# Kernel tuning notes

Hardware: AMD Instinct MI355X
Metric: run time of the kernel (lower is better)

The kernel has to match this reference:

```python
import jax, jax.numpy as jnp
import numpy as np

NH = 16   # num_heads
HD = 128  # head_dim
HS = 2048 # hidden_size
LI, LT = 2048, 512
MLP = 4 * HS


def _ln(x, s, b):
    m = jnp.mean(x, axis=-1, keepdims=True)
    v = jnp.var(x, axis=-1, keepdims=True)
    return (x - m) * jax.lax.rsqrt(v + 1e-6) * s + b


def _rms(x, s):
    return x * jax.lax.rsqrt(jnp.mean(x * x, axis=-1, keepdims=True) + 1e-6) * s


def _mod6(vec, w, b):
    a = (jax.nn.silu(vec) @ w + b)[:, None, :]
    return jnp.split(a, 6, axis=-1)  # shift1,scale1,gate1,shift2,scale2,gate2


def _rope(x, pe):
    B, H, L, D = x.shape
    xr = x.reshape(B, H, L, D // 2, 1, 2)
    return (pe[..., 0] * xr[..., 0] + pe[..., 1] * xr[..., 1]).reshape(B, H, L, D)


def _attention(q, k, v, pe):
    q = _rope(q, pe)
    k = _rope(k, pe)
    scores = jnp.einsum('bhqd,bhkd->bhqk', q, k) * (q.shape[-1] ** -0.5)
    p = jax.nn.softmax(scores, axis=-1)
    o = jnp.einsum('bhqk,bhkd->bhqd', p, v)
    B, H, L, D = o.shape
    return o.transpose(0, 2, 1, 3).reshape(B, L, H * D)


def _prenorm_qkv(x, shift, scale, ln_s, ln_b, qkv_w, qkv_b, qn, kn):
    xm = (1.0 + scale) * _ln(x, ln_s, ln_b) + shift
    y = xm @ qkv_w + qkv_b
    B, L, _ = y.shape
    y = y.reshape(B, L, 3, NH, HD).transpose(2, 0, 3, 1, 4)  # K B H L D
    q, k, v = y[0], y[1], y[2]
    return _rms(q, qn), _rms(k, kn), v


def _forward(img, txt, vec, pe,
             img_mod_w, img_mod_b, img_norm1_s, img_norm1_b, img_qkv_w, img_qkv_b,
             img_qn_s, img_kn_s, img_proj_w, img_proj_b, img_norm2_s, img_norm2_b,
             img_mlp_w1, img_mlp_b1, img_mlp_w2, img_mlp_b2,
             txt_mod_w, txt_mod_b, txt_norm1_s, txt_norm1_b, txt_qkv_w, txt_qkv_b,
             txt_qn_s, txt_kn_s, txt_proj_w, txt_proj_b, txt_norm2_s, txt_norm2_b,
             txt_mlp_w1, txt_mlp_b1, txt_mlp_w2, txt_mlp_b2):
    i_sh1, i_sc1, i_g1, i_sh2, i_sc2, i_g2 = _mod6(vec, img_mod_w, img_mod_b)
    t_sh1, t_sc1, t_g1, t_sh2, t_sc2, t_g2 = _mod6(vec, txt_mod_w, txt_mod_b)

    iq, ik, iv = _prenorm_qkv(img, i_sh1, i_sc1, img_norm1_s, img_norm1_b,
                              img_qkv_w, img_qkv_b, img_qn_s, img_kn_s)
    tq, tk, tv = _prenorm_qkv(txt, t_sh1, t_sc1, txt_norm1_s, txt_norm1_b,
                              txt_qkv_w, txt_qkv_b, txt_qn_s, txt_kn_s)

    q = jnp.concatenate((tq, iq), axis=2)
    k = jnp.concatenate((tk, ik), axis=2)
    v = jnp.concatenate((tv, iv), axis=2)
    attn = _attention(q, k, v, pe)  # [B, LT+LI, HS]
    Lt = txt.shape[1]
    txt_attn, img_attn = attn[:, :Lt], attn[:, Lt:]

    img = img + i_g1 * (img_attn @ img_proj_w + img_proj_b)
    img_h = (1.0 + i_sc2) * _ln(img, img_norm2_s, img_norm2_b) + i_sh2
    img = img + i_g2 * (jax.nn.gelu(img_h @ img_mlp_w1 + img_mlp_b1) @ img_mlp_w2 + img_mlp_b2)

    txt = txt + t_g1 * (txt_attn @ txt_proj_w + txt_proj_b)
    txt_h = (1.0 + t_sc2) * _ln(txt, txt_norm2_s, txt_norm2_b) + t_sh2
    txt = txt + t_g2 * (jax.nn.gelu(txt_h @ txt_mlp_w1 + txt_mlp_b1) @ txt_mlp_w2 + txt_mlp_b2)
    return img, txt


def setup_inputs() -> dict:
    key = jax.random.key(0)
    ki = iter(jax.random.split(key, 48))
    def n(shape, s=0.02):
        return jax.random.normal(next(ki), shape, jnp.float32) * s
    d = {
        'img': jax.random.normal(next(ki), (1, LI, HS), jnp.float32),
        'txt': jax.random.normal(next(ki), (1, LT, HS), jnp.float32),
        'vec': jax.random.normal(next(ki), (1, HS), jnp.float32),
        'pe': jax.random.normal(next(ki), (1, 1, LT + LI, HD // 2, 2, 2), jnp.float32),
    }
    for p in ('img', 'txt'):
        d[p + '_mod_w'] = n((HS, 6 * HS)); d[p + '_mod_b'] = jnp.zeros((6 * HS,), jnp.float32)
        d[p + '_norm1_s'] = jnp.ones((HS,), jnp.float32); d[p + '_norm1_b'] = jnp.zeros((HS,), jnp.float32)
        d[p + '_qkv_w'] = n((HS, 3 * HS)); d[p + '_qkv_b'] = jnp.zeros((3 * HS,), jnp.float32)
        d[p + '_qn_s'] = jnp.ones((HD,), jnp.float32); d[p + '_kn_s'] = jnp.ones((HD,), jnp.float32)
        d[p + '_proj_w'] = n((HS, HS)); d[p + '_proj_b'] = jnp.zeros((HS,), jnp.float32)
        d[p + '_norm2_s'] = jnp.ones((HS,), jnp.float32); d[p + '_norm2_b'] = jnp.zeros((HS,), jnp.float32)
        d[p + '_mlp_w1'] = n((HS, MLP)); d[p + '_mlp_b1'] = jnp.zeros((MLP,), jnp.float32)
        d[p + '_mlp_w2'] = n((MLP, HS)); d[p + '_mlp_b2'] = jnp.zeros((HS,), jnp.float32)
    return d


def reference(img, txt, vec, pe,
              img_mod_w, img_mod_b, img_norm1_s, img_norm1_b, img_qkv_w, img_qkv_b,
              img_qn_s, img_kn_s, img_proj_w, img_proj_b, img_norm2_s, img_norm2_b,
              img_mlp_w1, img_mlp_b1, img_mlp_w2, img_mlp_b2,
              txt_mod_w, txt_mod_b, txt_norm1_s, txt_norm1_b, txt_qkv_w, txt_qkv_b,
              txt_qn_s, txt_kn_s, txt_proj_w, txt_proj_b, txt_norm2_s, txt_norm2_b,
              txt_mlp_w1, txt_mlp_b1, txt_mlp_w2, txt_mlp_b2):
    return _forward(img, txt, vec, pe,
                    img_mod_w, img_mod_b, img_norm1_s, img_norm1_b, img_qkv_w, img_qkv_b,
                    img_qn_s, img_kn_s, img_proj_w, img_proj_b, img_norm2_s, img_norm2_b,
                    img_mlp_w1, img_mlp_b1, img_mlp_w2, img_mlp_b2,
                    txt_mod_w, txt_mod_b, txt_norm1_s, txt_norm1_b, txt_qkv_w, txt_qkv_b,
                    txt_qn_s, txt_kn_s, txt_proj_w, txt_proj_b, txt_norm2_s, txt_norm2_b,
                    txt_mlp_w1, txt_mlp_b1, txt_mlp_w2, txt_mlp_b2)
```

## Files before the change

### kernel.cpp

```cpp
#include <hip/hip_runtime.h>
#include <hip/hip_bf16.h>
#include <math.h>

typedef __bf16 bf16;
typedef __bf16 bf16x2 __attribute__((ext_vector_type(2)));
typedef __bf16 bf16x4 __attribute__((ext_vector_type(4)));
typedef __bf16 bf16x8 __attribute__((ext_vector_type(8)));
typedef float f32x4 __attribute__((ext_vector_type(4)));

#define HS 2048
#define NH 16
#define HD 128
#define LT 512
#define LI 2048
#define LQ 2560
#define MLP_D 8192
#define SPLIT 4
#define KVS (LQ / SPLIT)
#define KVBLK 32
#define NTILES (KVS / KVBLK)

__device__ __forceinline__ f32x4 mfma16(bf16x8 a, bf16x8 b, f32x4 c) {
  return __builtin_amdgcn_mfma_f32_16x16x32_bf16(a, b, c, 0, 0, 0);
}

__device__ __forceinline__ void gl_lds16(const bf16* g, bf16* l) {
  __builtin_amdgcn_global_load_lds((const __attribute__((address_space(1))) void*)g,
                                   (__attribute__((address_space(3))) void*)l, 16, 0, 0);
}

__global__ void k_silu(const float* __restrict__ v, float* __restrict__ s) {
  int i = blockIdx.x * 256 + threadIdx.x;
  float x = v[i];
  s[i] = x / (1.f + expf(-x));
}

__global__ __launch_bounds__(256) void k_mod_partial(
    const float* __restrict__ s, const float* __restrict__ w_txt,
    const float* __restrict__ w_img, float* __restrict__ part) {
  int strm = blockIdx.x / 48;
  int n = (blockIdx.x % 48) * 256 + threadIdx.x;
  const float* w = strm ? w_img : w_txt;
  int k0 = blockIdx.y * 256;
  __shared__ float sl[256];
  sl[threadIdx.x] = s[k0 + threadIdx.x];
  __syncthreads();
  float acc = 0.f;
  for (int k = 0; k < 256; k++)
    acc += sl[k] * w[(size_t)(k0 + k) * 12288 + n];
  part[((size_t)blockIdx.y * 2 + strm) * 12288 + n] = acc;
}

__global__ __launch_bounds__(256) void k_mod_reduce(
    const float* __restrict__ part, const float* __restrict__ b_txt,
    const float* __restrict__ b_img, float* __restrict__ mod) {
  int strm = blockIdx.x / 48;
  int n = (blockIdx.x % 48) * 256 + threadIdx.x;
  float acc = strm ? b_img[n] : b_txt[n];
  for (int kc = 0; kc < 8; kc++)
    acc += part[((size_t)kc * 2 + strm) * 12288 + n];
  mod[(size_t)strm * 12288 + n] = acc;
}

__global__ __launch_bounds__(256) void k_transpose_cvt(
    const float* __restrict__ src, bf16* __restrict__ dst, int R, int C) {
  __shared__ float t[64][65];
  int tx = threadIdx.x & 63, ty = threadIdx.x >> 6;
  int c0 = blockIdx.x * 64, r0 = blockIdx.y * 64;
  for (int i = 0; i < 64; i += 4)
    t[ty + i][tx] = src[(size_t)(r0 + ty + i) * C + c0 + tx];
  __syncthreads();
#pragma unroll
  for (int j = 0; j < 2; j++) {
    int c = (threadIdx.x >> 3) + j * 32;
    int gg = (threadIdx.x & 7) * 8;
    bf16x8 ov;
#pragma unroll
    for (int k = 0; k < 8; k++) ov[k] = (bf16)t[gg + k][c];
    *(bf16x8*)(dst + (size_t)(c0 + c) * R + r0 + gg) = ov;
  }
}

__global__ __launch_bounds__(256) void k_ln_mod(
    const float* __restrict__ x0, const float* __restrict__ x1,
    const float* __restrict__ ls0, const float* __restrict__ lb0,
    const float* __restrict__ ls1, const float* __restrict__ lb1,
    const float* __restrict__ mod0, const float* __restrict__ mod1,
    int shidx, int scidx, bf16* __restrict__ out) {
  int r = blockIdx.x;
  int strm = r >= LT;
  const float* x = strm ? (x1 + (size_t)(r - LT) * HS) : (x0 + (size_t)r * HS);
  const float* ls = strm ? ls1 : ls0;
  const float* lb = strm ? lb1 : lb0;
  const float* md = strm ? mod1 : mod0;
  const float* sh = md + (size_t)shidx * HS;
  const float* sc = md + (size_t)scidx * HS;
  int t = threadIdx.x;
  float4 a = ((const float4*)x)[t * 2];
  float4 b = ((const float4*)x)[t * 2 + 1];
  float xv[8] = {a.x, a.y, a.z, a.w, b.x, b.y, b.z, b.w};
  float sum = 0.f, sq = 0.f;
#pragma unroll
  for (int j = 0; j < 8; j++) { sum += xv[j]; sq += xv[j] * xv[j]; }
#pragma unroll
  for (int m = 32; m; m >>= 1) { sum += __shfl_xor(sum, m); sq += __shfl_xor(sq, m); }
  __shared__ float red[8];
  int lane = t & 63, wid = t >> 6;
  if (!lane) { red[wid] = sum; red[wid + 4] = sq; }
  __syncthreads();
  float ts = red[0] + red[1] + red[2] + red[3];
  float tq = red[4] + red[5] + red[6] + red[7];
  float mean = ts * (1.f / HS);
  float var = tq * (1.f / HS) - mean * mean;
  float inv = rsqrtf(var + 1e-6f);
  int c0 = t * 8;
  bf16x8 ov;
#pragma unroll
  for (int j = 0; j < 8; j++) {
    int c = c0 + j;
    float v = ((xv[j] - mean) * inv * ls[c] + lb[c]) * (1.f + sc[c]) + sh[c];
    ov[j] = (bf16)v;
  }
  *(bf16x8*)(out + (size_t)r * HS + c0) = ov;
}

template <int MODE>
__global__ __launch_bounds__(256) void k_gemm(
    const bf16* __restrict__ A, int K, int N, int Ksz,
    const bf16* __restrict__ BT0, const bf16* __restrict__ BT1,
    const float* __restrict__ bias0, const float* __restrict__ bias1,
    void* __restrict__ out0, void* __restrict__ out1) {
  __shared__ bf16 As[2][128 * 32];
  __shared__ bf16 Bs[2][128 * 32];
  int tid = threadIdx.x;
  int bn = blockIdx.x, bm = blockIdx.y;
  int strm = (bm * 128) >= LT;
  int lm = bm * 128 - strm * LT;
  const bf16* BT = strm ? BT1 : BT0;
  int lane = tid & 63, wid = tid >> 6;
  int wr = wid >> 1, wc = wid & 1;
  int sr = tid >> 2;
  int scol = ((tid & 3) ^ (sr & 3)) * 8;
  const bf16* Ag = A + (size_t)(bm * 128 + sr) * K + scol;
  const bf16* Bg = BT + (size_t)(bn * 128 + sr) * K + scol;
  int kbeg = MODE == 4 ? blockIdx.z * Ksz : 0;
  int nk = Ksz / 32;
  auto stage = [&](int buf, int ks) {
    int k0 = kbeg + ks * 32;
    gl_lds16(Ag + k0, &As[buf][wid * 512]);
    gl_lds16(Ag + (size_t)64 * K + k0, &As[buf][2048 + wid * 512]);
    gl_lds16(Bg + k0, &Bs[buf][wid * 512]);
    gl_lds16(Bg + (size_t)64 * K + k0, &Bs[buf][2048 + wid * 512]);
  };
  f32x4 acc[4][4] = {};
  int r16 = lane & 15, g = lane >> 4;
  int fslot = (g ^ (r16 & 3)) * 8;
  stage(0, 0);
  int cur = 0;
  for (int ks = 0; ks < nk; ks++) {
    __syncthreads();
    if (ks + 1 < nk) stage(cur ^ 1, ks + 1);
    bf16x8 af[4], bfr[4];
#pragma unroll
    for (int m = 0; m < 4; m++)
      af[m] = *(const bf16x8*)&As[cur][(wr * 64 + m * 16 + r16) * 32 + fslot];
#pragma unroll
    for (int n = 0; n < 4; n++)
      bfr[n] = *(const bf16x8*)&Bs[cur][(wc * 64 + n * 16 + r16) * 32 + fslot];
#pragma unroll
    for (int m = 0; m < 4; m++)
#pragma unroll
      for (int n = 0; n < 4; n++)
        acc[m][n] = mfma16(af[m], bfr[n], acc[m][n]);
    cur ^= 1;
  }
  int col = lane & 15, rb = (lane >> 4) * 4;
  const float* bias = strm ? bias1 : bias0;
  float* part = MODE == 4 ? (float*)out0 + (size_t)blockIdx.z * LQ * N : nullptr;
#pragma unroll
  for (int m = 0; m < 4; m++) {
#pragma unroll
    for (int n = 0; n < 4; n++) {
      int gn = bn * 128 + wc * 64 + n * 16 + col;
      float bv = MODE == 4 ? 0.f : bias[gn];
#pragma unroll
      for (int r = 0; r < 4; r++) {
        int lr = wr * 64 + m * 16 + rb + r;
        float v = acc[m][n][r] + bv;
        if (MODE == 0) {
          ((bf16*)(strm ? out1 : out0))[(size_t)(lm + lr) * N + gn] = (bf16)v;
        } else if (MODE == 2) {
          float u2 = 1.5957691216057308f * (v + 0.044715f * v * v * v);
          float ge = v / (1.f + __expf(-u2));
          ((bf16*)(strm ? out1 : out0))[(size_t)(lm + lr) * N + gn] = (bf16)ge;
        } else {
          part[(size_t)(bm * 128 + lr) * N + gn] = v;
        }
      }
    }
  }
}

template <int S>
__global__ __launch_bounds__(256) void k_skcomb(
    const float* __restrict__ part, int N,
    const float* __restrict__ bias0, const float* __restrict__ bias1,
    const float* __restrict__ gate0, const float* __restrict__ gate1,
    const float* __restrict__ res0, const float* __restrict__ res1,
    float* __restrict__ out0, float* __restrict__ out1) {
  int gid = blockIdx.x * 256 + threadIdx.x;
  int nv = N >> 2;
  int row = gid / nv, cv = gid - row * nv;
  int strm = row >= LT;
  int lrow = row - strm * LT;
  const float* bias = strm ? bias1 : bias0;
  const float* gate = strm ? gate1 : gate0;
  const float* res = strm ? res1 : res0;
  float* out = strm ? out1 : out0;
  int c = cv * 4;
  float4 acc = *(const float4*)(bias + c);
#pragma unroll
  for (int s = 0; s < S; s++) {
    float4 p = *(const float4*)(part + ((size_t)s * LQ + row) * N + c);
    acc.x += p.x; acc.y += p.y; acc.z += p.z; acc.w += p.w;
  }
  float4 g = *(const float4*)(gate + c);
  float4 r = *(const float4*)(res + (size_t)lrow * N + c);
  float4 o = {r.x + g.x * acc.x, r.y + g.y * acc.y, r.z + g.z * acc.z, r.w + g.w * acc.w};
  *(float4*)(out + (size_t)lrow * N + c) = o;
}

__global__ __launch_bounds__(256) void k_qkv_post(
    const bf16* __restrict__ y, const float* __restrict__ pe,
    const float* __restrict__ qn0, const float* __restrict__ kn0,
    const float* __restrict__ qn1, const float* __restrict__ kn1,
    bf16* __restrict__ qh, bf16* __restrict__ kh) {
  int wv = (int)((blockIdx.x * 256 + threadIdx.x) >> 6);
  int lane = threadIdx.x & 63;
  int head = wv / LQ, l = wv - head * LQ;
  const bf16* yr = y + (size_t)l * (3 * HS) + head * HD;
  float q0 = (float)yr[2 * lane], q1 = (float)yr[2 * lane + 1];
  float k0 = (float)yr[HS + 2 * lane], k1 = (float)yr[HS + 2 * lane + 1];
  float sqs = q0 * q0 + q1 * q1, sks = k0 * k0 + k1 * k1;
#pragma unroll
  for (int m = 1; m < 64; m <<= 1) { sqs += __shfl_xor(sqs, m); sks += __shfl_xor(sks, m); }
  float rq = rsqrtf(sqs * (1.f / HD) + 1e-6f);
  float rk = rsqrtf(sks * (1.f / HD) + 1e-6f);
  int strm = l >= LT;
  const float* qn = strm ? qn1 : qn0;
  const float* kn = strm ? kn1 : kn0;
  float e0 = q0 * rq * qn[2 * lane], e1 = q1 * rq * qn[2 * lane + 1];
  float f0 = k0 * rk * kn[2 * lane], f1 = k1 * rk * kn[2 * lane + 1];
  float4 p = *(const float4*)(pe + ((size_t)l * 64 + lane) * 4);
  const float scl = 0.12751744f;
  size_t qi = ((size_t)head * LQ + l) * HD + 2 * lane;
  bf16x2 qv = {(bf16)((p.x * e0 + p.y * e1) * scl), (bf16)((p.z * e0 + p.w * e1) * scl)};
  bf16x2 kv = {(bf16)(p.x * f0 + p.y * f1), (bf16)(p.z * f0 + p.w * f1)};
  *(bf16x2*)(qh + qi) = qv;
  *(bf16x2*)(kh + qi) = kv;
}

__global__ __launch_bounds__(256) void k_vtrans(const bf16* __restrict__ y,
                                                bf16* __restrict__ vT) {
  __shared__ bf16 t[32][34];
  int head = blockIdx.y >> 2, dt = blockIdx.y & 3;
  int tx = threadIdx.x & 31, ty = threadIdx.x >> 5;
  int l0 = blockIdx.x * 32, d0 = dt * 32;
  for (int i = 0; i < 32; i += 8)
    t[ty + i][tx] = y[(size_t)(l0 + ty + i) * (3 * HS) + 2 * HS + head * HD + d0 + tx];
  __syncthreads();
  for (int i = 0; i < 32; i += 8)
    vT[(size_t)(head * HD + d0 + ty + i) * LQ + l0 + tx] = t[tx][ty + i];
}

__global__ __launch_bounds__(256, 5) void k_attn(
    const bf16* __restrict__ Q, const bf16* __restrict__ Kh,
    const bf16* __restrict__ VT, bf16* __restrict__ Op, float* __restrict__ ml) {
  __shared__ bf16 Ks[2][KVBLK * 128];
  __shared__ bf16 Vs[2][128 * KVBLK];
  int tid = threadIdx.x, lane = tid & 63, w = tid >> 6;
  int b = blockIdx.x;
  int qb = b % 40;
  int split = (b / 40) % SPLIT;
  int head = b / (40 * SPLIT);
  int qr = qb * 64 + w * 16;
  int r16 = lane & 15, g = lane >> 4;
  const bf16* qp = Q + ((size_t)head * LQ + qr + r16) * HD + g * 8;
  bf16x8 qf[4];
#pragma unroll
  for (int c = 0; c < 4; c++) qf[c] = *(const bf16x8*)(qp + c * 32);
  f32x4 O[8] = {};
  float mr = -1e30f, lr = 0.f;
  const bf16* kbase = Kh + ((size_t)head * LQ + split * KVS) * HD;
  const bf16* vbase = VT + (size_t)head * HD * LQ + split * KVS;
  int krow0 = w * 8 + (lane >> 4);
  int kslot = lane & 15;
  int vrow0 = w * 32 + (lane >> 2);
  int vslot = lane & 3;
  auto stage = [&](int buf, int t) {
    int kv0 = t * KVBLK;
#pragma unroll
    for (int i = 0; i < 2; i++) {
      int krow = krow0 + i * 4;
      gl_lds16(kbase + (size_t)(kv0 + krow) * HD + ((kslot ^ (krow & 7)) << 3),
               &Ks[buf][(w * 8 + i * 4) * 128]);
      int vrow = vrow0 + i * 16;
      gl_lds16(vbase + (size_t)vrow * LQ + kv0 + ((vslot ^ (vrow & 3)) << 3),
               &Vs[buf][(w * 32 + i * 16) * KVBLK]);
    }
  };
  stage(0, 0);
  int cur = 0;
  int src0 = r16 + ((g & 1) << 5);
  bool hiS = g >= 2;
  for (int t = 0; t < NTILES; t++) {
    __syncthreads();
    if (t + 1 < NTILES) stage(cur ^ 1, t + 1);
    const bf16* ks = &Ks[cur][0];
    const bf16* vs = &Vs[cur][0];
    f32x4 S0 = {}, S1 = {};
    int sw = (r16 & 7);
#pragma unroll
    for (int c = 0; c < 4; c++) {
      int slot = ((4 * c + g) ^ sw) << 3;
      bf16x8 ka = *(const bf16x8*)&ks[r16 * 128 + slot];
      bf16x8 kb = *(const bf16x8*)&ks[(16 + r16) * 128 + slot];
      S0 = mfma16(ka, qf[c], S0);
      S1 = mfma16(kb, qf[c], S1);
    }
    float mx = fmaxf(fmaxf(fmaxf(S0[0], S0[1]), fmaxf(S0[2], S0[3])),
                     fmaxf(fmaxf(S1[0], S1[1]), fmaxf(S1[2], S1[3])));
    mx = fmaxf(mx, __shfl_xor(mx, 16));
    mx = fmaxf(mx, __shfl_xor(mx, 32));
    bool keep = __all(mx <= mr + 8.f);
    float alpha = 1.f;
    if (!keep) {
      float mn = fmaxf(mr, mx);
      alpha = exp2f(mr - mn);
      mr = mn;
    }
    float p0 = exp2f(S0[0] - mr), p1 = exp2f(S0[1] - mr);
    float p2 = exp2f(S0[2] - mr), p3 = exp2f(S0[3] - mr);
    float p4 = exp2f(S1[0] - mr), p5 = exp2f(S1[1] - mr);
    float p6 = exp2f(S1[2] - mr), p7 = exp2f(S1[3] - mr);
    float rs = ((p0 + p1) + (p2 + p3)) + ((p4 + p5) + (p6 + p7));
    rs += __shfl_xor(rs, 16);
    rs += __shfl_xor(rs, 32);
    lr = fmaf(lr, alpha, rs);
    bf16x2 a0 = {(bf16)p0, (bf16)p1}, a1 = {(bf16)p2, (bf16)p3};
    bf16x2 b0 = {(bf16)p4, (bf16)p5}, b1 = {(bf16)p6, (bf16)p7};
    int A0 = *(int*)&a0, A1 = *(int*)&a1, B0 = *(int*)&b0, B1 = *(int*)&b1;
    int x0a = __shfl(A0, src0), x0b = __shfl(B0, src0);
    int x1a = __shfl(A1, src0), x1b = __shfl(B1, src0);
    int x2a = __shfl(A0, src0 + 16), x2b = __shfl(B0, src0 + 16);
    int x3a = __shfl(A1, src0 + 16), x3b = __shfl(B1, src0 + 16);
    union { int u[4]; bf16x8 v; } pu;
    pu.u[0] = hiS ? x0b : x0a;
    pu.u[1] = hiS ? x1b : x1a;
    pu.u[2] = hiS ? x2b : x2a;
    pu.u[3] = hiS ? x3b : x3a;
    bf16x8 pf = pu.v;
    if (!keep) {
#pragma unroll
      for (int n = 0; n < 8; n++) O[n] *= alpha;
    }
    int vsl = (g ^ (r16 & 3)) * 8;
#pragma unroll
    for (int n = 0; n < 8; n++) {
      bf16x8 vf = *(const bf16x8*)&vs[(n * 16 + r16) * KVBLK + vsl];
      O[n] = mfma16(vf, pf, O[n]);
    }
    cur ^= 1;
  }
  const int NL = NH * LQ;
  bf16* op = Op + (size_t)split * NL * HD;
  size_t rowbase = ((size_t)head * LQ + qr + r16) * HD + 4 * g;
#pragma unroll
  for (int n = 0; n < 8; n++) {
    bf16x4 ov = {(bf16)O[n][0], (bf16)O[n][1], (bf16)O[n][2], (bf16)O[n][3]};
    *(bf16x4*)(op + rowbase + n * 16) = ov;
  }
  if (g == 0) {
    int idx = head * LQ + qr + r16;
    ml[(size_t)(split * 2 + 0) * NL + idx] = mr;
    ml[(size_t)(split * 2 + 1) * NL + idx] = lr;
  }
}

__global__ __launch_bounds__(256) void k_attn_combine(
    const bf16* __restrict__ Op, const float* __restrict__ ml, bf16* __restrict__ out) {
  int lane = threadIdx.x & 63, w = threadIdx.x >> 6;
  int row = blockIdx.x * 4 + w;
  int head = row / LQ, l = row - head * LQ;
  const int NL = NH * LQ;
  float ms[SPLIT], ls[SPLIT], m = -1e30f;
#pragma unroll
  for (int s = 0; s < SPLIT; s++) {
    ms[s] = ml[(size_t)(s * 2) * NL + row];
    ls[s] = ml[(size_t)(s * 2 + 1) * NL + row];
    m = fmaxf(m, ms[s]);
  }
  float wsum = 0.f, wgt[SPLIT];
#pragma unroll
  for (int s = 0; s < SPLIT; s++) { wgt[s] = exp2f(ms[s] - m); wsum += wgt[s] * ls[s]; }
  float inv = 1.f / wsum;
  size_t oi = (size_t)row * HD + 2 * lane;
  float a0 = 0.f, a1 = 0.f;
#pragma unroll
  for (int s = 0; s < SPLIT; s++) {
    bf16x2 v = *(const bf16x2*)(Op + (size_t)s * NL * HD + oi);
    a0 += wgt[s] * (float)v[0];
    a1 += wgt[s] * (float)v[1];
  }
  bf16x2 ov = {(bf16)(a0 * inv), (bf16)(a1 * inv)};
  *(bf16x2*)(out + (size_t)l * HS + head * HD + 2 * lane) = ov;
}

extern "C" void kernel_launch(void* const* d_in, const int* in_sizes, int n_in,
                              void* d_out, int out_size, void* d_ws, size_t ws_size,
                              hipStream_t stream) {
  const float* img = (const float*)d_in[0];
  const float* txt = (const float*)d_in[1];
  const float* vec = (const float*)d_in[2];
  const float* pe = (const float*)d_in[3];
#define PARAM(i) ((const float*)d_in[i])

  char* ws = (char*)d_ws;
  size_t off = 0;
  auto alloc = [&](size_t b) { void* p = ws + off; off += (b + 255) & ~(size_t)255; return p; };
  float* silu_s = (float*)alloc((size_t)HS * 4);
  float* mpart = (float*)alloc((size_t)8 * 2 * 12288 * 4);
  float* mod = (float*)alloc((size_t)2 * 6 * HS * 4);
  bf16* qkvT0 = (bf16*)alloc((size_t)3 * HS * HS * 2);
  bf16* qkvT1 = (bf16*)alloc((size_t)3 * HS * HS * 2);
  bf16* projT0 = (bf16*)alloc((size_t)HS * HS * 2);
  bf16* projT1 = (bf16*)alloc((size_t)HS * HS * 2);
  bf16* mlp1T0 = (bf16*)alloc((size_t)MLP_D * HS * 2);
  bf16* mlp1T1 = (bf16*)alloc((size_t)MLP_D * HS * 2);
  bf16* mlp2T0 = (bf16*)alloc((size_t)HS * MLP_D * 2);
  bf16* mlp2T1 = (bf16*)alloc((size_t)HS * MLP_D * 2);
  bf16* xm = (bf16*)alloc((size_t)LQ * HS * 2);
  bf16* y = (bf16*)alloc((size_t)LQ * 3 * HS * 2);
  bf16* qh = (bf16*)alloc((size_t)NH * LQ * HD * 2);
  bf16* kh = (bf16*)alloc((size_t)NH * LQ * HD * 2);
  bf16* vT = (bf16*)alloc((size_t)NH * HD * LQ * 2);
  bf16* attnb = (bf16*)alloc((size_t)LQ * HS * 2);
  float* x2 = (float*)alloc((size_t)LQ * HS * 4);
  bf16* xm2 = (bf16*)alloc((size_t)LQ * HS * 2);
  bf16* h = (bf16*)alloc((size_t)LQ * MLP_D * 2);
  float* ml = (float*)alloc((size_t)2 * SPLIT * NH * LQ * 4);
  bf16* Op = h;
  float* skpart = (float*)xm;
  (void)ws_size; (void)in_sizes; (void)n_in; (void)out_size;

  const float* t_mod = mod;
  const float* i_mod = mod + 6 * HS;

  k_silu<<<HS / 256, 256, 0, stream>>>(vec, silu_s);
  k_mod_partial<<<dim3(96, 8), 256, 0, stream>>>(silu_s, PARAM(20), PARAM(4), mpart);
  k_mod_reduce<<<96, 256, 0, stream>>>(mpart, PARAM(21), PARAM(5), mod);

  k_transpose_cvt<<<dim3(3 * HS / 64, HS / 64), 256, 0, stream>>>(PARAM(24), qkvT0, HS, 3 * HS);
  k_transpose_cvt<<<dim3(3 * HS / 64, HS / 64), 256, 0, stream>>>(PARAM(8), qkvT1, HS, 3 * HS);
  k_transpose_cvt<<<dim3(HS / 64, HS / 64), 256, 0, stream>>>(PARAM(28), projT0, HS, HS);
  k_transpose_cvt<<<dim3(HS / 64, HS / 64), 256, 0, stream>>>(PARAM(12), projT1, HS, HS);
  k_transpose_cvt<<<dim3(MLP_D / 64, HS / 64), 256, 0, stream>>>(PARAM(32), mlp1T0, HS, MLP_D);
  k_transpose_cvt<<<dim3(MLP_D / 64, HS / 64), 256, 0, stream>>>(PARAM(16), mlp1T1, HS, MLP_D);
  k_transpose_cvt<<<dim3(HS / 64, MLP_D / 64), 256, 0, stream>>>(PARAM(34), mlp2T0, MLP_D, HS);
  k_transpose_cvt<<<dim3(HS / 64, MLP_D / 64), 256, 0, stream>>>(PARAM(18), mlp2T1, MLP_D, HS);

  k_ln_mod<<<LQ, 256, 0, stream>>>(txt, img, PARAM(22), PARAM(23), PARAM(6), PARAM(7),
                                   t_mod, i_mod, 0, 1, xm);

  k_gemm<0><<<dim3(3 * HS / 128, LQ / 128), 256, 0, stream>>>(
      xm, HS, 3 * HS, HS, qkvT0, qkvT1, PARAM(25), PARAM(9), y, y + (size_t)LT * 3 * HS);

  k_qkv_post<<<NH * LQ / 4, 256, 0, stream>>>(y, pe, PARAM(26), PARAM(27), PARAM(10), PARAM(11),
                                              qh, kh);
  k_vtrans<<<dim3(LQ / 32, NH * 4), 256, 0, stream>>>(y, vT);

  k_attn<<<NH * SPLIT * 40, 256, 0, stream>>>(qh, kh, vT, Op, ml);
  k_attn_combine<<<NH * LQ / 4, 256, 0, stream>>>(Op, ml, attnb);

  k_gemm<4><<<dim3(HS / 128, LQ / 128, 2), 256, 0, stream>>>(
      attnb, HS, HS, HS / 2, projT0, projT1, nullptr, nullptr, skpart, nullptr);
  k_skcomb<2><<<LQ * HS / 4 / 256, 256, 0, stream>>>(
      skpart, HS, PARAM(29), PARAM(13), t_mod + 2 * HS, i_mod + 2 * HS, txt, img,
      x2, x2 + (size_t)LT * HS);

  k_ln_mod<<<LQ, 256, 0, stream>>>(x2, x2 + (size_t)LT * HS, PARAM(30), PARAM(31), PARAM(14),
                                   PARAM(15), t_mod, i_mod, 3, 4, xm2);

  k_gemm<2><<<dim3(MLP_D / 128, LQ / 128), 256, 0, stream>>>(
      xm2, HS, MLP_D, HS, mlp1T0, mlp1T1, PARAM(33), PARAM(17), h, h + (size_t)LT * MLP_D);

  float* out_img = (float*)d_out;
  float* out_txt = (float*)d_out + (size_t)LI * HS;
  k_gemm<4><<<dim3(HS / 128, LQ / 128, 4), 256, 0, stream>>>(
      h, MLP_D, HS, MLP_D / 4, mlp2T0, mlp2T1, nullptr, nullptr, skpart, nullptr);
  k_skcomb<4><<<LQ * HS / 4 / 256, 256, 0, stream>>>(
      skpart, HS, PARAM(35), PARAM(19), t_mod + 5 * HS, i_mod + 5 * HS, x2,
      x2 + (size_t)LT * HS, out_txt, out_img);
}
```

Baseline: 763.1 us.

## Add 128x256 GEMM kernel with 64-wide K tiles and XOR-swizzled LDS

Adds a new GEMM kernel with 512 threads that computes 128x256 output tiles. Each K step is 64 wide and is staged into LDS through an XOR-swizzled layout, which is meant to avoid bank conflicts. The QKV, MLP1 and MLP2 GEMMs now use this kernel, so each block gets more reuse from every tile load and runs fewer K-loop syncs. The old kernel is cut down to the split-K projection path only. In exchange, the grid has fewer blocks and each one uses more LDS (96KB double-buffered), which may lower occupancy.

```diff
diff --git a/kernel.cpp b/kernel.cpp
--- a/kernel.cpp
+++ b/kernel.cpp
@@ -122,6 +122,95 @@
     ov[j] = (bf16)v;
   }
   *(bf16x8*)(out + (size_t)r * HS + c0) = ov;
+}
+
+template <int MODE>
+__global__ __launch_bounds__(512, 2) void k_gemm256(
+    const bf16* __restrict__ A, int K, int N, int Ksz,
+    const bf16* __restrict__ BT0, const bf16* __restrict__ BT1,
+    const float* __restrict__ bias0, const float* __restrict__ bias1,
+    void* __restrict__ out0, void* __restrict__ out1) {
+  __shared__ bf16 As[2][128 * 64];
+  __shared__ bf16 Bs[2][256 * 64];
+  int tid = threadIdx.x;
+  int bn = blockIdx.x, bm = blockIdx.y;
+  int strm = (bm * 128) >= LT;
+  int lm = bm * 128 - strm * LT;
+  const bf16* BT = strm ? BT1 : BT0;
+  int lane = tid & 63, wid = tid >> 6;
+  int wr = wid >> 2, wc = wid & 3;
+  int srow = tid >> 3;
+  int col8 = (((tid & 7) ^ (srow & 7)) << 3);
+  const bf16* Ag = A + (size_t)(bm * 128 + srow) * K + col8;
+  const bf16* Bg = BT + (size_t)(bn * 256 + srow) * K + col8;
+  int kbeg = MODE == 4 ? blockIdx.z * Ksz : 0;
+  int nk = Ksz / 64;
+  auto stage = [&](int buf, int kt) {
+    int k0 = kbeg + kt * 64;
+#pragma unroll
+    for (int j = 0; j < 2; j++)
+      gl_lds16(Ag + (size_t)(j * 64) * K + k0, &As[buf][j * 4096 + tid * 8]);
+#pragma unroll
+    for (int j = 0; j < 4; j++)
+      gl_lds16(Bg + (size_t)(j * 64) * K + k0, &Bs[buf][j * 4096 + tid * 8]);
+  };
+  f32x4 acc[4][4] = {};
+  int r16 = lane & 15, g = lane >> 4;
+  int sa = r16 & 7;
+  stage(0, 0);
+  int cur = 0;
+  for (int kt = 0; kt < nk; kt++) {
+    __syncthreads();
+    if (kt + 1 < nk) stage(cur ^ 1, kt + 1);
+    bf16x8 af[4][2], bfr[4][2];
+#pragma unroll
+    for (int m = 0; m < 4; m++) {
+      int ar = wr * 64 + m * 16 + r16;
+#pragma unroll
+      for (int kk = 0; kk < 2; kk++)
+        af[m][kk] = *(const bf16x8*)&As[cur][ar * 64 + (((kk * 4 + g) ^ sa) << 3)];
+    }
+#pragma unroll
+    for (int n = 0; n < 4; n++) {
+      int br = wc * 64 + n * 16 + r16;
+#pragma unroll
+      for (int kk = 0; kk < 2; kk++)
+        bfr[n][kk] = *(const bf16x8*)&Bs[cur][br * 64 + (((kk * 4 + g) ^ sa) << 3)];
+    }
+#pragma unroll
+    for (int kk = 0; kk < 2; kk++)
+#pragma unroll
+      for (int m = 0; m < 4; m++)
+#pragma unroll
+        for (int n = 0; n < 4; n++)
+          acc[m][n] = mfma16(af[m][kk], bfr[n][kk], acc[m][n]);
+    cur ^= 1;
+  }
+  int col = lane & 15, rb = (lane >> 4) * 4;
+  const float* bias = strm ? bias1 : bias0;
+  float* part = MODE == 4 ? (float*)out0 + (size_t)blockIdx.z * LQ * N : nullptr;
+#pragma unroll
+  for (int m = 0; m < 4; m++) {
+#pragma unroll
+    for (int n = 0; n < 4; n++) {
+      int gn = bn * 256 + wc * 64 + n * 16 + col;
+      float bv = MODE == 4 ? 0.f : bias[gn];
+#pragma unroll
+      for (int r = 0; r < 4; r++) {
+        int lr = wr * 64 + m * 16 + rb + r;
+        float v = acc[m][n][r] + bv;
+        if (MODE == 0) {
+          ((bf16*)(strm ? out1 : out0))[(size_t)(lm + lr) * N + gn] = (bf16)v;
+        } else if (MODE == 2) {
+          float u2 = 1.5957691216057308f * (v + 0.044715f * v * v * v);
+          float ge = v / (1.f + __expf(-u2));
+          ((bf16*)(strm ? out1 : out0))[(size_t)(lm + lr) * N + gn] = (bf16)ge;
+        } else {
+          part[(size_t)(bm * 128 + lr) * N + gn] = v;
+        }
+      }
+    }
+  }
 }
 
 template <int MODE>
@@ -175,30 +264,20 @@
     cur ^= 1;
   }
   int col = lane & 15, rb = (lane >> 4) * 4;
-  const float* bias = strm ? bias1 : bias0;
-  float* part = MODE == 4 ? (float*)out0 + (size_t)blockIdx.z * LQ * N : nullptr;
+  float* part = (float*)out0 + (size_t)blockIdx.z * LQ * N;
 #pragma unroll
   for (int m = 0; m < 4; m++) {
 #pragma unroll
     for (int n = 0; n < 4; n++) {
       int gn = bn * 128 + wc * 64 + n * 16 + col;
-      float bv = MODE == 4 ? 0.f : bias[gn];
 #pragma unroll
       for (int r = 0; r < 4; r++) {
         int lr = wr * 64 + m * 16 + rb + r;
-        float v = acc[m][n][r] + bv;
-        if (MODE == 0) {
-          ((bf16*)(strm ? out1 : out0))[(size_t)(lm + lr) * N + gn] = (bf16)v;
-        } else if (MODE == 2) {
-          float u2 = 1.5957691216057308f * (v + 0.044715f * v * v * v);
-          float ge = v / (1.f + __expf(-u2));
-          ((bf16*)(strm ? out1 : out0))[(size_t)(lm + lr) * N + gn] = (bf16)ge;
-        } else {
-          part[(size_t)(bm * 128 + lr) * N + gn] = v;
-        }
+        part[(size_t)(bm * 128 + lr) * N + gn] = acc[m][n][r];
       }
     }
   }
+  (void)bias0; (void)bias1; (void)out1; (void)lm;
 }
 
 template <int S>
@@ -472,7 +551,7 @@
   k_ln_mod<<<LQ, 256, 0, stream>>>(txt, img, PARAM(22), PARAM(23), PARAM(6), PARAM(7),
                                    t_mod, i_mod, 0, 1, xm);
 
-  k_gemm<0><<<dim3(3 * HS / 128, LQ / 128), 256, 0, stream>>>(
+  k_gemm256<0><<<dim3(3 * HS / 256, LQ / 128), 512, 0, stream>>>(
       xm, HS, 3 * HS, HS, qkvT0, qkvT1, PARAM(25), PARAM(9), y, y + (size_t)LT * 3 * HS);
 
   k_qkv_post<<<NH * LQ / 4, 256, 0, stream>>>(y, pe, PARAM(26), PARAM(27), PARAM(10), PARAM(11),
@@ -491,12 +570,12 @@
   k_ln_mod<<<LQ, 256, 0, stream>>>(x2, x2 + (size_t)LT * HS, PARAM(30), PARAM(31), PARAM(14),
                                    PARAM(15), t_mod, i_mod, 3, 4, xm2);
 
-  k_gemm<2><<<dim3(MLP_D / 128, LQ / 128), 256, 0, stream>>>(
+  k_gemm256<2><<<dim3(MLP_D / 256, LQ / 128), 512, 0, stream>>>(
       xm2, HS, MLP_D, HS, mlp1T0, mlp1T1, PARAM(33), PARAM(17), h, h + (size_t)LT * MLP_D);
 
   float* out_img = (float*)d_out;
   float* out_txt = (float*)d_out + (size_t)LI * HS;
-  k_gemm<4><<<dim3(HS / 128, LQ / 128, 4), 256, 0, stream>>>(
+  k_gemm256<4><<<dim3(HS / 256, LQ / 128, 4), 512, 0, stream>>>(
       h, MLP_D, HS, MLP_D / 4, mlp2T0, mlp2T1, nullptr, nullptr, skpart, nullptr);
   k_skcomb<4><<<LQ * HS / 4 / 256, 256, 0, stream>>>(
       skpart, HS, PARAM(35), PARAM(19), t_mod + 5 * HS, i_mod + 5 * HS, x2,
```

New measurement: 814.5 us. 1.07x slower.
